# Performance work log

Hardware: AMD Instinct MI355X
Metric: run time of the kernel (lower is better)

The kernel has to match this reference:

```python
import jax, jax.numpy as jnp
import numpy as np

C = 256
CQK = C // 8  # reduction_ratio = 8


def setup_inputs() -> dict:
    key = jax.random.key(0)
    ks = jax.random.split(key, 8)
    B, H, W = 8, 64, 64
    x = jax.random.normal(ks[0], (B, C, H, W), dtype=jnp.float32)
    s_in = 1.0 / np.sqrt(C)
    Wq = jax.random.normal(ks[1], (CQK, C), dtype=jnp.float32) * s_in
    bq = jax.random.normal(ks[2], (CQK,), dtype=jnp.float32) * 0.01
    Wk = jax.random.normal(ks[3], (CQK, C), dtype=jnp.float32) * s_in
    bk = jax.random.normal(ks[4], (CQK,), dtype=jnp.float32) * 0.01
    Wv = jax.random.normal(ks[5], (C, C), dtype=jnp.float32) * s_in
    bv = jax.random.normal(ks[6], (C,), dtype=jnp.float32) * 0.01
    gamma = jax.random.normal(ks[7], (1,), dtype=jnp.float32) * 0.1
    return {"x": x, "Wq": Wq, "bq": bq, "Wk": Wk, "bk": bk,
            "Wv": Wv, "bv": bv, "gamma": gamma}


def reference(x, Wq, bq, Wk, bk, Wv, bv, gamma):
    B, Cc, H, W = x.shape
    N = H * W
    xf = x.reshape(B, Cc, N)  # [B, C, N]
    # 1x1 convs == per-pixel linear maps over channels
    q = jnp.einsum('qc,bcn->bnq', Wq, xf) + bq            # [B, N, Cqk]
    k = jnp.einsum('kc,bcn->bkn', Wk, xf) + bk[None, :, None]  # [B, Cqk, N]
    v = jnp.einsum('vc,bcn->bvn', Wv, xf) + bv[None, :, None]  # [B, C, N]
    # unscaled attention scores, softmax over keys (last dim)
    scores = jax.nn.softmax(jnp.einsum('bnq,bqm->bnm', q, k), axis=-1)  # [B, N, N]
    # out[b,c,n] = sum_m v[b,c,m] * scores[b,n,m]  (torch: value @ scores^T)
    attn = jnp.einsum('bvm,bnm->bvn', v, scores)          # [B, C, N]
    out = gamma[0] * attn.reshape(B, Cc, H, W) + x
    return out
```

## Files before the change

### kernel.cpp

```cpp
#include <hip/hip_runtime.h>

static constexpr int B_   = 8;
static constexpr int C_   = 256;
static constexpr int CQK_ = 32;
static constexpr int N_   = 4096;

typedef __attribute__((ext_vector_type(4)))  float f32x4;
typedef __attribute__((ext_vector_type(16))) float f32x16;
typedef __attribute__((ext_vector_type(8)))  short short8;
typedef __attribute__((ext_vector_type(2)))  unsigned int u32x2;
typedef unsigned short ushort_t;

__device__ inline unsigned short f2bf(float f) {
    unsigned u = __float_as_uint(f);
    return (unsigned short)((u + 0x7FFFu + ((u >> 16) & 1u)) >> 16);
}
__device__ inline unsigned packbf(float lo, float hi) {
    return (unsigned)f2bf(lo) | ((unsigned)f2bf(hi) << 16);
}
__device__ inline unsigned cvtpk(float lo, float hi) {
    unsigned r;
    asm("v_cvt_pk_bf16_f32 %0, %1, %2" : "=v"(r) : "v"(lo), "v"(hi));
    return r;
}
__device__ inline float vexp2(float x) {
    float r;
    asm("v_exp_f32 %0, %1" : "=v"(r) : "v"(x));
    return r;
}
__device__ inline void plswap(unsigned& a, unsigned& b) {
    asm("v_permlane32_swap_b32 %0, %1" : "+v"(a), "+v"(b));
}

__device__ inline int swzbits(int m) {
    return ((m & 3) << 5) | (((m >> 3) & 1) << 4);
}

template <int OFF>
__device__ inline u32x2 tr8(unsigned a) {
    u32x2 d;
    asm volatile("ds_read_b64_tr_b16 %0, %1 offset:%2"
                 : "=v"(d) : "v"(a), "i"(OFF));
    return d;
}

__device__ inline short8 mk8(u32x2 lo, u32x2 hi) {
    union { unsigned u[4]; short8 s; } v;
    v.u[0] = lo.x; v.u[1] = lo.y; v.u[2] = hi.x; v.u[3] = hi.y;
    return v.s;
}
__device__ inline short8 mk8u(unsigned a, unsigned b, unsigned c, unsigned d) {
    union { unsigned u[4]; short8 s; } v;
    v.u[0] = a; v.u[1] = b; v.u[2] = c; v.u[3] = d;
    return v.s;
}

__global__ __launch_bounds__(256) void prep_kernel(
    const float* __restrict__ Wq, const float* __restrict__ bq,
    const float* __restrict__ Wk, const float* __restrict__ bk,
    const float* __restrict__ Wv, const float* __restrict__ bv,
    ushort_t* __restrict__ Wall, float* __restrict__ ball)
{
    const int r = blockIdx.x;
    const int t = threadIdx.x;
    const float LOG2E = 1.4426950408889634f;
    const float* src;
    float bsrc, sc;
    if (r < 32)      { src = Wq + (size_t)r * C_;        bsrc = bq[r];      sc = LOG2E; }
    else if (r < 64) { src = Wk + (size_t)(r - 32) * C_; bsrc = bk[r - 32]; sc = 1.0f; }
    else             { src = Wv + (size_t)(r - 64) * C_; bsrc = bv[r - 64]; sc = 1.0f; }
    Wall[(size_t)r * C_ + t] = f2bf(src[t] * sc);
    if (t == 0) ball[r] = bsrc * sc;
}

__global__ __launch_bounds__(256) void proj_kernel(
    const float* __restrict__ x,
    const ushort_t* __restrict__ Wall, const float* __restrict__ ball,
    ushort_t* __restrict__ Qb, ushort_t* __restrict__ Kb, ushort_t* __restrict__ Vt)
{
    __shared__ __align__(16) unsigned char xs[C_ * 128];
    typedef __attribute__((address_space(3))) unsigned char lds_byte;
    const unsigned sbase = (unsigned)(size_t)(lds_byte*)xs;

    const int b  = blockIdx.x & 7;
    const int n0 = (blockIdx.x >> 3) << 6;
    const int t  = threadIdx.x;

    {
        const int cst = t >> 4;
        const int n4  = (t & 15) << 2;
        const float* xb = x + (size_t)b * C_ * N_ + n0;
        #pragma unroll
        for (int i = 0; i < 16; ++i) {
            const int c = 16 * i + cst;
            float4 v = *(const float4*)(xb + (size_t)c * N_ + n4);
            u32x2 pk;
            pk.x = packbf(v.x, v.y);
            pk.y = packbf(v.z, v.w);
            *(u32x2*)(xs + c * 128 + ((n4 * 2) ^ swzbits(c))) = pk;
        }
    }
    __syncthreads();

    const int l  = t & 63, w = t >> 6;
    const int li = l & 15, g = l >> 4;
    const int rr = li >> 2, ss = l & 3;
    const int swz_tr = (rr << 5) | ((g & 1) << 4);

    f32x4 acc[5][4];
    #pragma unroll
    for (int i = 0; i < 5; ++i)
        #pragma unroll
        for (int j = 0; j < 4; ++j) acc[i][j] = (f32x4){0.f, 0.f, 0.f, 0.f};

    #pragma unroll 2
    for (int kg = 0; kg < 8; ++kg) {
        u32x2 pb[4][2];
        #pragma unroll
        for (int jn = 0; jn < 4; ++jn) {
            unsigned a = sbase + (32 * kg + 8 * g + rr) * 128
                       + ((32 * jn + 8 * ss) ^ swz_tr);
            pb[jn][0] = tr8<0>(a);
            pb[jn][1] = tr8<512>(a);
        }
        short8 af[5];
        #pragma unroll
        for (int tm = 0; tm < 5; ++tm)
            af[tm] = *(const short8*)(Wall + (size_t)(16 * (4 * tm + w) + li) * C_
                                      + 32 * kg + 8 * g);
        asm volatile("s_waitcnt lgkmcnt(0)" ::: "memory");
        __builtin_amdgcn_sched_barrier(0);
        #pragma unroll
        for (int jn = 0; jn < 4; ++jn) {
            short8 Bf = mk8(pb[jn][0], pb[jn][1]);
            acc[0][jn] = __builtin_amdgcn_mfma_f32_16x16x32_bf16(
                             af[0], Bf, acc[0][jn], 0, 0, 0);
            #pragma unroll
            for (int tm = 1; tm < 5; ++tm)
                acc[tm][jn] = __builtin_amdgcn_mfma_f32_16x16x32_bf16(
                                  Bf, af[tm], acc[tm][jn], 0, 0, 0);
        }
    }

    {
        const int oc0 = 16 * w + 4 * g;
        float4 bias = *(const float4*)(ball + oc0);
        ushort_t* dst = (w < 2) ? Qb : Kb;
        const int col = (w < 2) ? oc0 : (oc0 - 32);
        #pragma unroll
        for (int jn = 0; jn < 4; ++jn) {
            const int n = n0 + 16 * jn + li;
            f32x4 a = acc[0][jn];
            u32x2 pk;
            pk.x = packbf(a[0] + bias.x, a[1] + bias.y);
            pk.y = packbf(a[2] + bias.z, a[3] + bias.w);
            *(u32x2*)(dst + (size_t)(b * N_ + n) * CQK_ + col) = pk;
        }
    }
    {
        const int sx = (li & 7) << 4;
        #pragma unroll
        for (int tm = 1; tm < 5; ++tm) {
            const int c  = 16 * (4 * tm + w) + li - 64;
            const float bc = ball[64 + c];
            char* vrow = (char*)Vt
                       + ((size_t)(b * 64 + (n0 >> 6)) * 256 + c) * 128;
            #pragma unroll
            for (int jn = 0; jn < 4; ++jn) {
                f32x4 a = acc[tm][jn];
                u32x2 pk;
                pk.x = packbf(a[0] + bc, a[1] + bc);
                pk.y = packbf(a[2] + bc, a[3] + bc);
                *(u32x2*)(vrow + ((32 * jn + 8 * g) ^ sx)) = pk;
            }
        }
    }
}

__global__ __launch_bounds__(256, 2) void attn_kernel(
    const float* __restrict__ x,
    const ushort_t* __restrict__ Qb, const ushort_t* __restrict__ Kb,
    const ushort_t* __restrict__ Vt,
    const float* __restrict__ gamma, float* __restrict__ out)
{
    __shared__ __align__(16) unsigned char smem[66560];

    const int b   = blockIdx.x & 7;
    const int n0  = (blockIdx.x >> 3) << 6;
    const int t   = threadIdx.x;
    const int l   = t & 63, w = t >> 6;
    const int l31 = l & 31, h2 = l >> 5;
    const int sxv = (l & 7) << 4;
    unsigned char* wlds = smem + w * 16384;
    float* rslw = (float*)(smem + 65536) + w * 64;

    short8 qfv[2][2];
    #pragma unroll
    for (int jq = 0; jq < 2; ++jq)
        #pragma unroll
        for (int kh = 0; kh < 2; ++kh)
            qfv[jq][kh] = *(const short8*)(Qb
                + (size_t)(b * N_ + n0 + 32 * jq + l31) * CQK_ + 16 * kh + 8 * h2);

    f32x16 acc[2][2];
    #pragma unroll
    for (int i = 0; i < 2; ++i)
        #pragma unroll
        for (int j = 0; j < 2; ++j)
            #pragma unroll
            for (int e = 0; e < 16; ++e) acc[i][j][e] = 0.f;
    float rs[2] = {0.f, 0.f};

    const ushort_t* Kbb = Kb + (size_t)(b * N_) * CQK_;
    const char* Vgb = (const char*)Vt + (size_t)b * 64 * 32768 + w * 8192;

    short8 kfA[2][2], kfB[2][2];

    #pragma unroll
    for (int jm = 0; jm < 2; ++jm)
        #pragma unroll
        for (int kh = 0; kh < 2; ++kh)
            kfA[jm][kh] = *(const short8*)(Kbb
                + (size_t)(32 * jm + l31) * CQK_ + 16 * kh + 8 * h2);
    #pragma unroll
    for (int i = 0; i < 8; ++i)
        __builtin_amdgcn_global_load_lds(
            (const __attribute__((address_space(1))) unsigned int*)(Vgb + l * 16 + i * 1024),
            (__attribute__((address_space(3))) unsigned int*)(wlds + l * 16 + i * 1024),
            16, 0, 0);

#define CHUNK_BODY(CH, KFC, KFN)                                                \
    {                                                                           \
        const int chn = ((CH) + 1) & 63;                                        \
                                                         \
        _Pragma("unroll")                                                       \
        for (int jm = 0; jm < 2; ++jm)                                          \
            _Pragma("unroll")                                                   \
            for (int kh = 0; kh < 2; ++kh)                                      \
                KFN[jm][kh] = *(const short8*)(Kbb                              \
                    + (size_t)(64 * chn + 32 * jm + l31) * CQK_                 \
                    + 16 * kh + 8 * h2);                                        \
                                 \
        {                                                                       \
            const char* gsrc = Vgb + (size_t)chn * 32768 + l * 16;              \
            unsigned char* ldst = wlds + (((CH) + 1) & 1) * 8192 + l * 16;      \
            _Pragma("unroll")                                                   \
            for (int i = 0; i < 8; ++i)                                         \
                __builtin_amdgcn_global_load_lds(                               \
                    (const __attribute__((address_space(1))) unsigned int*)(gsrc + i * 1024), \
                    (__attribute__((address_space(3))) unsigned int*)(ldst + i * 1024), \
                    16, 0, 0);                                                  \
        }                                                                       \
            \
        unsigned paw[4][2][4];                                                  \
        _Pragma("unroll")                                                       \
        for (int jm = 0; jm < 2; ++jm) {                                        \
            _Pragma("unroll")                                                   \
            for (int jq = 0; jq < 2; ++jq) {                                    \
                f32x16 sv;                                                      \
                _Pragma("unroll")                                               \
                for (int e = 0; e < 16; ++e) sv[e] = 0.f;                       \
                sv = __builtin_amdgcn_mfma_f32_32x32x16_bf16(                   \
                         KFC[jm][0], qfv[jq][0], sv, 0, 0, 0);                  \
                sv = __builtin_amdgcn_mfma_f32_32x32x16_bf16(                   \
                         KFC[jm][1], qfv[jq][1], sv, 0, 0, 0);                  \
                float ev[16];                                                   \
                _Pragma("unroll")                                               \
                for (int e = 0; e < 16; ++e) ev[e] = vexp2(sv[e]);              \
                float sm = ((ev[0] + ev[1]) + (ev[2] + ev[3]))                  \
                         + ((ev[4] + ev[5]) + (ev[6] + ev[7]))                  \
                         + ((ev[8] + ev[9]) + (ev[10] + ev[11]))                \
                         + ((ev[12] + ev[13]) + (ev[14] + ev[15]));             \
                rs[jq] += sm;                                                   \
                unsigned u0 = cvtpk(ev[0], ev[1]),   u1 = cvtpk(ev[2], ev[3]);  \
                unsigned u2 = cvtpk(ev[4], ev[5]),   u3 = cvtpk(ev[6], ev[7]);  \
                unsigned u4 = cvtpk(ev[8], ev[9]),   u5 = cvtpk(ev[10], ev[11]);\
                unsigned u6 = cvtpk(ev[12], ev[13]), u7 = cvtpk(ev[14], ev[15]);\
                plswap(u0, u2); plswap(u1, u3);                                 \
                plswap(u4, u6); plswap(u5, u7);                                 \
                paw[2 * jm + 0][jq][0] = u0; paw[2 * jm + 0][jq][1] = u1;       \
                paw[2 * jm + 0][jq][2] = u2; paw[2 * jm + 0][jq][3] = u3;       \
                paw[2 * jm + 1][jq][0] = u4; paw[2 * jm + 1][jq][1] = u5;       \
                paw[2 * jm + 1][jq][2] = u6; paw[2 * jm + 1][jq][3] = u7;       \
            }                                                                   \
        }                                                                       \
                \
        asm volatile("s_waitcnt vmcnt(12)" ::: "memory");                       \
                           \
        {                                                                       \
            const unsigned char* vb = wlds + ((CH) & 1) * 8192;                 \
            short8 vv[2][4];                                                    \
            _Pragma("unroll")                                                   \
            for (int jc = 0; jc < 2; ++jc)                                      \
                _Pragma("unroll")                                               \
                for (int s = 0; s < 4; ++s)                                     \
                    vv[jc][s] = *(const short8*)(vb + (32 * jc + l31) * 128     \
                                   + ((32 * s + 16 * h2) ^ sxv));               \
            _Pragma("unroll")                                                   \
            for (int jq = 0; jq < 2; ++jq)                                      \
                _Pragma("unroll")                                               \
                for (int jc = 0; jc < 2; ++jc)                                  \
                    _Pragma("unroll")                                           \
                    for (int s = 0; s < 4; ++s)                                 \
                        acc[jq][jc] = __builtin_amdgcn_mfma_f32_32x32x16_bf16(  \
                            mk8u(paw[s][jq][0], paw[s][jq][1],                  \
                                 paw[s][jq][2], paw[s][jq][3]),                 \
                            vv[jc][s], acc[jq][jc], 0, 0, 0);                   \
        }                                                                       \
    }

    for (int mc = 0; mc < 64; mc += 2) {
        CHUNK_BODY(mc,     kfA, kfB)
        CHUNK_BODY(mc + 1, kfB, kfA)
    }
#undef CHUNK_BODY

    #pragma unroll
    for (int jq = 0; jq < 2; ++jq)
        rs[jq] += __shfl_xor(rs[jq], 32, 64);
    if (l < 32) {
        rslw[l]      = rs[0];
        rslw[32 + l] = rs[1];
    }
    asm volatile("s_waitcnt lgkmcnt(0)" ::: "memory");

    const float gm = gamma[0];
    #pragma unroll
    for (int jq = 0; jq < 2; ++jq)
        #pragma unroll
        for (int rg = 0; rg < 4; ++rg) {
            f32x4 sv = *(const f32x4*)(rslw + 32 * jq + 8 * rg + 4 * h2);
            float i0 = 1.0f / sv[0], i1 = 1.0f / sv[1];
            float i2 = 1.0f / sv[2], i3 = 1.0f / sv[3];
            const int n = n0 + 32 * jq + 8 * rg + 4 * h2;
            #pragma unroll
            for (int jc = 0; jc < 2; ++jc) {
                const int c = 64 * w + 32 * jc + l31;
                const size_t rowoff = (size_t)(b * C_ + c) * N_ + n;
                float4 xv = *(const float4*)(x + rowoff);
                float4 o;
                o.x = gm * acc[jq][jc][4 * rg + 0] * i0 + xv.x;
                o.y = gm * acc[jq][jc][4 * rg + 1] * i1 + xv.y;
                o.z = gm * acc[jq][jc][4 * rg + 2] * i2 + xv.z;
                o.w = gm * acc[jq][jc][4 * rg + 3] * i3 + xv.w;
                *(float4*)(out + rowoff) = o;
            }
        }
}

extern "C" void kernel_launch(void* const* d_in, const int* in_sizes, int n_in,
                              void* d_out, int out_size, void* d_ws, size_t ws_size,
                              hipStream_t stream)
{
    const float* x     = (const float*)d_in[0];
    const float* Wq    = (const float*)d_in[1];
    const float* bq    = (const float*)d_in[2];
    const float* Wk    = (const float*)d_in[3];
    const float* bk    = (const float*)d_in[4];
    const float* Wv    = (const float*)d_in[5];
    const float* bv    = (const float*)d_in[6];
    const float* gamma = (const float*)d_in[7];
    float* out = (float*)d_out;

    ushort_t* ws = (ushort_t*)d_ws;
    ushort_t* Qb   = ws;
    ushort_t* Kb   = Qb + (size_t)B_ * N_ * CQK_;
    ushort_t* Vt   = Kb + (size_t)B_ * N_ * CQK_;
    ushort_t* Wall = Vt + (size_t)B_ * C_ * N_;
    float*    ball = (float*)(Wall + (size_t)320 * C_);

    prep_kernel<<<320, 256, 0, stream>>>(Wq, bq, Wk, bk, Wv, bv, Wall, ball);
    proj_kernel<<<B_ * (N_ / 64), 256, 0, stream>>>(x, Wall, ball, Qb, Kb, Vt);
    attn_kernel<<<B_ * (N_ / 64), 256, 0, stream>>>(x, Qb, Kb, Vt, gamma, out);
}
```

Measured before the change: 150.6 us.

## Halve attention query tile to 32 and re-layout V into 32-key chunks

The attention kernel now handles 32 queries per block instead of 64 and iterates over 128 key chunks of 32 instead of 64 chunks of 64. The grid doubles, LDS and register use per block halve, and the launch-bounds occupancy hint is dropped. The projection kernel writes V in a matching 32-key chunk layout with a new XOR swizzle. This trades reuse of each K/V chunk across queries, so K/V traffic and per-chunk overhead double, for more blocks and higher occupancy to hide latency.

```diff
diff --git a/kernel.cpp b/kernel.cpp
--- a/kernel.cpp
+++ b/kernel.cpp
@@ -157,73 +157,69 @@
             *(u32x2*)(dst + (size_t)(b * N_ + n) * CQK_ + col) = pk;
         }
     }
-    {
-        const int sx = (li & 7) << 4;
-        #pragma unroll
-        for (int tm = 1; tm < 5; ++tm) {
-            const int c  = 16 * (4 * tm + w) + li - 64;
-            const float bc = ball[64 + c];
-            char* vrow = (char*)Vt
-                       + ((size_t)(b * 64 + (n0 >> 6)) * 256 + c) * 128;
-            #pragma unroll
-            for (int jn = 0; jn < 4; ++jn) {
-                f32x4 a = acc[tm][jn];
-                u32x2 pk;
-                pk.x = packbf(a[0] + bc, a[1] + bc);
-                pk.y = packbf(a[2] + bc, a[3] + bc);
-                *(u32x2*)(vrow + ((32 * jn + 8 * g) ^ sx)) = pk;
-            }
-        }
-    }
-}
-
-__global__ __launch_bounds__(256, 2) void attn_kernel(
+    #pragma unroll
+    for (int tm = 1; tm < 5; ++tm) {
+        const int c  = 16 * (4 * tm + w) + li - 64;
+        const float bc = ball[64 + c];
+        const int sxc = ((c >> 1) & 3) << 4;
+        #pragma unroll
+        for (int jn = 0; jn < 4; ++jn) {
+            const int ch = (n0 >> 5) + (jn >> 1);
+            const int mcol = 32 * (jn & 1) + 8 * g;
+            f32x4 a = acc[tm][jn];
+            u32x2 pk;
+            pk.x = packbf(a[0] + bc, a[1] + bc);
+            pk.y = packbf(a[2] + bc, a[3] + bc);
+            char* dst = (char*)Vt + (size_t)(b * 128 + ch) * 16384
+                      + c * 64 + (mcol ^ sxc);
+            *(u32x2*)dst = pk;
+        }
+    }
+}
+
+__global__ __launch_bounds__(256) void attn_kernel(
     const float* __restrict__ x,
     const ushort_t* __restrict__ Qb, const ushort_t* __restrict__ Kb,
     const ushort_t* __restrict__ Vt,
     const float* __restrict__ gamma, float* __restrict__ out)
 {
-    __shared__ __align__(16) unsigned char smem[66560];
+    __shared__ __align__(16) unsigned char smem[33280];
 
     const int b   = blockIdx.x & 7;
-    const int n0  = (blockIdx.x >> 3) << 6;
+    const int n0  = (blockIdx.x >> 3) << 5;
     const int t   = threadIdx.x;
     const int l   = t & 63, w = t >> 6;
     const int l31 = l & 31, h2 = l >> 5;
-    const int sxv = (l & 7) << 4;
-    unsigned char* wlds = smem + w * 16384;
-    float* rslw = (float*)(smem + 65536) + w * 64;
-
-    short8 qfv[2][2];
-    #pragma unroll
-    for (int jq = 0; jq < 2; ++jq)
-        #pragma unroll
-        for (int kh = 0; kh < 2; ++kh)
-            qfv[jq][kh] = *(const short8*)(Qb
-                + (size_t)(b * N_ + n0 + 32 * jq + l31) * CQK_ + 16 * kh + 8 * h2);
-
-    f32x16 acc[2][2];
-    #pragma unroll
-    for (int i = 0; i < 2; ++i)
-        #pragma unroll
-        for (int j = 0; j < 2; ++j)
-            #pragma unroll
-            for (int e = 0; e < 16; ++e) acc[i][j][e] = 0.f;
-    float rs[2] = {0.f, 0.f};
+    const int sxv = ((l31 >> 1) & 3) << 4;
+    unsigned char* wlds = smem + w * 8192;
+    float* rslw = (float*)(smem + 32768) + w * 32;
+
+    short8 qfv[2];
+    #pragma unroll
+    for (int kh = 0; kh < 2; ++kh)
+        qfv[kh] = *(const short8*)(Qb
+            + (size_t)(b * N_ + n0 + l31) * CQK_ + 16 * kh + 8 * h2);
+
+    f32x16 acc[2];
+    #pragma unroll
+    for (int j = 0; j < 2; ++j)
+        #pragma unroll
+        for (int e = 0; e < 16; ++e) acc[j][e] = 0.f;
+    f32x16 zf16;
+    #pragma unroll
+    for (int e = 0; e < 16; ++e) zf16[e] = 0.f;
+    float rs = 0.f;
 
     const ushort_t* Kbb = Kb + (size_t)(b * N_) * CQK_;
-    const char* Vgb = (const char*)Vt + (size_t)b * 64 * 32768 + w * 8192;
-
-    short8 kfA[2][2], kfB[2][2];
-
-    #pragma unroll
-    for (int jm = 0; jm < 2; ++jm)
-        #pragma unroll
-        for (int kh = 0; kh < 2; ++kh)
-            kfA[jm][kh] = *(const short8*)(Kbb
-                + (size_t)(32 * jm + l31) * CQK_ + 16 * kh + 8 * h2);
-    #pragma unroll
-    for (int i = 0; i < 8; ++i)
+    const char* Vgb = (const char*)Vt + (size_t)b * 128 * 16384 + w * 4096;
+
+    short8 kfA[2], kfB[2];
+
+    #pragma unroll
+    for (int kh = 0; kh < 2; ++kh)
+        kfA[kh] = *(const short8*)(Kbb + (size_t)l31 * CQK_ + 16 * kh + 8 * h2);
+    #pragma unroll
+    for (int i = 0; i < 4; ++i)
         __builtin_amdgcn_global_load_lds(
             (const __attribute__((address_space(1))) unsigned int*)(Vgb + l * 16 + i * 1024),
             (__attribute__((address_space(3))) unsigned int*)(wlds + l * 16 + i * 1024),
@@ -231,121 +227,98 @@
 
 #define CHUNK_BODY(CH, KFC, KFN)                                                \
     {                                                                           \
-        const int chn = ((CH) + 1) & 63;                                        \
+        const int chn = ((CH) + 1) & 127;                                       \
                                                          \
         _Pragma("unroll")                                                       \
-        for (int jm = 0; jm < 2; ++jm)                                          \
-            _Pragma("unroll")                                                   \
-            for (int kh = 0; kh < 2; ++kh)                                      \
-                KFN[jm][kh] = *(const short8*)(Kbb                              \
-                    + (size_t)(64 * chn + 32 * jm + l31) * CQK_                 \
-                    + 16 * kh + 8 * h2);                                        \
+        for (int kh = 0; kh < 2; ++kh)                                          \
+            KFN[kh] = *(const short8*)(Kbb                                      \
+                + (size_t)(32 * chn + l31) * CQK_ + 16 * kh + 8 * h2);          \
                                  \
         {                                                                       \
-            const char* gsrc = Vgb + (size_t)chn * 32768 + l * 16;              \
-            unsigned char* ldst = wlds + (((CH) + 1) & 1) * 8192 + l * 16;      \
+            const char* gsrc = Vgb + (size_t)chn * 16384 + l * 16;              \
+            unsigned char* ldst = wlds + (((CH) + 1) & 1) * 4096 + l * 16;      \
             _Pragma("unroll")                                                   \
-            for (int i = 0; i < 8; ++i)                                         \
+            for (int i = 0; i < 4; ++i)                                         \
                 __builtin_amdgcn_global_load_lds(                               \
                     (const __attribute__((address_space(1))) unsigned int*)(gsrc + i * 1024), \
                     (__attribute__((address_space(3))) unsigned int*)(ldst + i * 1024), \
                     16, 0, 0);                                                  \
         }                                                                       \
             \
-        unsigned paw[4][2][4];                                                  \
-        _Pragma("unroll")                                                       \
-        for (int jm = 0; jm < 2; ++jm) {                                        \
+        unsigned paw[2][4];                                                     \
+        {                                                                       \
+            f32x16 sv = __builtin_amdgcn_mfma_f32_32x32x16_bf16(                \
+                            KFC[0], qfv[0], zf16, 0, 0, 0);                     \
+            sv = __builtin_amdgcn_mfma_f32_32x32x16_bf16(                       \
+                     KFC[1], qfv[1], sv, 0, 0, 0);                              \
+            float ev[16];                                                       \
             _Pragma("unroll")                                                   \
-            for (int jq = 0; jq < 2; ++jq) {                                    \
-                f32x16 sv;                                                      \
-                _Pragma("unroll")                                               \
-                for (int e = 0; e < 16; ++e) sv[e] = 0.f;                       \
-                sv = __builtin_amdgcn_mfma_f32_32x32x16_bf16(                   \
-                         KFC[jm][0], qfv[jq][0], sv, 0, 0, 0);                  \
-                sv = __builtin_amdgcn_mfma_f32_32x32x16_bf16(                   \
-                         KFC[jm][1], qfv[jq][1], sv, 0, 0, 0);                  \
-                float ev[16];                                                   \
-                _Pragma("unroll")                                               \
-                for (int e = 0; e < 16; ++e) ev[e] = vexp2(sv[e]);              \
-                float sm = ((ev[0] + ev[1]) + (ev[2] + ev[3]))                  \
-                         + ((ev[4] + ev[5]) + (ev[6] + ev[7]))                  \
-                         + ((ev[8] + ev[9]) + (ev[10] + ev[11]))                \
-                         + ((ev[12] + ev[13]) + (ev[14] + ev[15]));             \
-                rs[jq] += sm;                                                   \
-                unsigned u0 = cvtpk(ev[0], ev[1]),   u1 = cvtpk(ev[2], ev[3]);  \
-                unsigned u2 = cvtpk(ev[4], ev[5]),   u3 = cvtpk(ev[6], ev[7]);  \
-                unsigned u4 = cvtpk(ev[8], ev[9]),   u5 = cvtpk(ev[10], ev[11]);\
-                unsigned u6 = cvtpk(ev[12], ev[13]), u7 = cvtpk(ev[14], ev[15]);\
-                plswap(u0, u2); plswap(u1, u3);                                 \
-                plswap(u4, u6); plswap(u5, u7);                                 \
-                paw[2 * jm + 0][jq][0] = u0; paw[2 * jm + 0][jq][1] = u1;       \
-                paw[2 * jm + 0][jq][2] = u2; paw[2 * jm + 0][jq][3] = u3;       \
-                paw[2 * jm + 1][jq][0] = u4; paw[2 * jm + 1][jq][1] = u5;       \
-                paw[2 * jm + 1][jq][2] = u6; paw[2 * jm + 1][jq][3] = u7;       \
-            }                                                                   \
+            for (int e = 0; e < 16; ++e) ev[e] = vexp2(sv[e]);                  \
+            rs += (((ev[0] + ev[1]) + (ev[2] + ev[3]))                          \
+                 + ((ev[4] + ev[5]) + (ev[6] + ev[7])))                         \
+                + (((ev[8] + ev[9]) + (ev[10] + ev[11]))                        \
+                 + ((ev[12] + ev[13]) + (ev[14] + ev[15])));                    \
+            unsigned u0 = cvtpk(ev[0], ev[1]),   u1 = cvtpk(ev[2], ev[3]);      \
+            unsigned u2 = cvtpk(ev[4], ev[5]),   u3 = cvtpk(ev[6], ev[7]);      \
+            unsigned u4 = cvtpk(ev[8], ev[9]),   u5 = cvtpk(ev[10], ev[11]);    \
+            unsigned u6 = cvtpk(ev[12], ev[13]), u7 = cvtpk(ev[14], ev[15]);    \
+            plswap(u0, u2); plswap(u1, u3);                                     \
+            plswap(u4, u6); plswap(u5, u7);                                     \
+            paw[0][0] = u0; paw[0][1] = u1; paw[0][2] = u2; paw[0][3] = u3;     \
+            paw[1][0] = u4; paw[1][1] = u5; paw[1][2] = u6; paw[1][3] = u7;     \
         }                                                                       \
                 \
-        asm volatile("s_waitcnt vmcnt(12)" ::: "memory");                       \
+        asm volatile("s_waitcnt vmcnt(6)" ::: "memory");                        \
                            \
         {                                                                       \
-            const unsigned char* vb = wlds + ((CH) & 1) * 8192;                 \
-            short8 vv[2][4];                                                    \
+            const unsigned char* vb = wlds + ((CH) & 1) * 4096;                 \
+            short8 vv[2][2];                                                    \
             _Pragma("unroll")                                                   \
             for (int jc = 0; jc < 2; ++jc)                                      \
                 _Pragma("unroll")                                               \
-                for (int s = 0; s < 4; ++s)                                     \
-                    vv[jc][s] = *(const short8*)(vb + (32 * jc + l31) * 128     \
+                for (int s = 0; s < 2; ++s)                                     \
+                    vv[jc][s] = *(const short8*)(vb + (32 * jc + l31) * 64      \
                                    + ((32 * s + 16 * h2) ^ sxv));               \
             _Pragma("unroll")                                                   \
-            for (int jq = 0; jq < 2; ++jq)                                      \
+            for (int jc = 0; jc < 2; ++jc)                                      \
                 _Pragma("unroll")                                               \
-                for (int jc = 0; jc < 2; ++jc)                                  \
-                    _Pragma("unroll")                                           \
-                    for (int s = 0; s < 4; ++s)                                 \
-                        acc[jq][jc] = __builtin_amdgcn_mfma_f32_32x32x16_bf16(  \
-                            mk8u(paw[s][jq][0], paw[s][jq][1],                  \
-                                 paw[s][jq][2], paw[s][jq][3]),                 \
-                            vv[jc][s], acc[jq][jc], 0, 0, 0);                   \
+                for (int s = 0; s < 2; ++s)                                     \
+                    acc[jc] = __builtin_amdgcn_mfma_f32_32x32x16_bf16(          \
+                        mk8u(paw[s][0], paw[s][1], paw[s][2], paw[s][3]),       \
+                        vv[jc][s], acc[jc], 0, 0, 0);                           \
         }                                                                       \
     }
 
-    for (int mc = 0; mc < 64; mc += 2) {
+    for (int mc = 0; mc < 128; mc += 2) {
         CHUNK_BODY(mc,     kfA, kfB)
         CHUNK_BODY(mc + 1, kfB, kfA)
     }
 #undef CHUNK_BODY
 
-    #pragma unroll
-    for (int jq = 0; jq < 2; ++jq)
-        rs[jq] += __shfl_xor(rs[jq], 32, 64);
-    if (l < 32) {
-        rslw[l]      = rs[0];
-        rslw[32 + l] = rs[1];
-    }
+    rs += __shfl_xor(rs, 32, 64);
+    if (l < 32) rslw[l31] = rs;
     asm volatile("s_waitcnt lgkmcnt(0)" ::: "memory");
 
     const float gm = gamma[0];
     #pragma unroll
-    for (int jq = 0; jq < 2; ++jq)
-        #pragma unroll
-        for (int rg = 0; rg < 4; ++rg) {
-            f32x4 sv = *(const f32x4*)(rslw + 32 * jq + 8 * rg + 4 * h2);
-            float i0 = 1.0f / sv[0], i1 = 1.0f / sv[1];
-            float i2 = 1.0f / sv[2], i3 = 1.0f / sv[3];
-            const int n = n0 + 32 * jq + 8 * rg + 4 * h2;
-            #pragma unroll
-            for (int jc = 0; jc < 2; ++jc) {
-                const int c = 64 * w + 32 * jc + l31;
-                const size_t rowoff = (size_t)(b * C_ + c) * N_ + n;
-                float4 xv = *(const float4*)(x + rowoff);
-                float4 o;
-                o.x = gm * acc[jq][jc][4 * rg + 0] * i0 + xv.x;
-                o.y = gm * acc[jq][jc][4 * rg + 1] * i1 + xv.y;
-                o.z = gm * acc[jq][jc][4 * rg + 2] * i2 + xv.z;
-                o.w = gm * acc[jq][jc][4 * rg + 3] * i3 + xv.w;
-                *(float4*)(out + rowoff) = o;
-            }
-        }
+    for (int rg = 0; rg < 4; ++rg) {
+        f32x4 sv = *(const f32x4*)(rslw + 8 * rg + 4 * h2);
+        float i0 = 1.0f / sv[0], i1 = 1.0f / sv[1];
+        float i2 = 1.0f / sv[2], i3 = 1.0f / sv[3];
+        const int n = n0 + 8 * rg + 4 * h2;
+        #pragma unroll
+        for (int jc = 0; jc < 2; ++jc) {
+            const int c = 64 * w + 32 * jc + l31;
+            const size_t rowoff = (size_t)(b * C_ + c) * N_ + n;
+            float4 xv = *(const float4*)(x + rowoff);
+            float4 o;
+            o.x = gm * acc[jc][4 * rg + 0] * i0 + xv.x;
+            o.y = gm * acc[jc][4 * rg + 1] * i1 + xv.y;
+            o.z = gm * acc[jc][4 * rg + 2] * i2 + xv.z;
+            o.w = gm * acc[jc][4 * rg + 3] * i3 + xv.w;
+            *(float4*)(out + rowoff) = o;
+        }
+    }
 }
 
 extern "C" void kernel_launch(void* const* d_in, const int* in_sizes, int n_in,
@@ -371,5 +344,5 @@
 
     prep_kernel<<<320, 256, 0, stream>>>(Wq, bq, Wk, bk, Wv, bv, Wall, ball);
     proj_kernel<<<B_ * (N_ / 64), 256, 0, stream>>>(x, Wall, ball, Qb, Kb, Vt);
-    attn_kernel<<<B_ * (N_ / 64), 256, 0, stream>>>(x, Qb, Kb, Vt, gamma, out);
-}
+    attn_kernel<<<B_ * (N_ / 32), 256, 0, stream>>>(x, Qb, Kb, Vt, gamma, out);
+}
```

Result: slower. 189.5 us (+25.9%).

## Split attention work across waves by key half instead of channel slice

Applied to the files above, without the earlier changes.

Each wave now takes half of each 64-key chunk and 128 output channels, instead of all keys and 64 channels. This halves the redundant QK^T MFMA and exp work per wave, since each score is computed once rather than by all four waves. The V layout written by the projection kernel changes to match, and the two key-halves are reduced through shared memory at the end. The cost is doubled accumulator registers (acc[2][4]), extra LDS traffic, two barriers, and an epilogue handled by only half the waves.

```diff
diff --git a/kernel.cpp b/kernel.cpp
--- a/kernel.cpp
+++ b/kernel.cpp
@@ -157,22 +157,25 @@
             *(u32x2*)(dst + (size_t)(b * N_ + n) * CQK_ + col) = pk;
         }
     }
-    {
-        const int sx = (li & 7) << 4;
-        #pragma unroll
-        for (int tm = 1; tm < 5; ++tm) {
-            const int c  = 16 * (4 * tm + w) + li - 64;
-            const float bc = ball[64 + c];
-            char* vrow = (char*)Vt
-                       + ((size_t)(b * 64 + (n0 >> 6)) * 256 + c) * 128;
-            #pragma unroll
-            for (int jn = 0; jn < 4; ++jn) {
-                f32x4 a = acc[tm][jn];
-                u32x2 pk;
-                pk.x = packbf(a[0] + bc, a[1] + bc);
-                pk.y = packbf(a[2] + bc, a[3] + bc);
-                *(u32x2*)(vrow + ((32 * jn + 8 * g) ^ sx)) = pk;
-            }
+    #pragma unroll
+    for (int tm = 1; tm < 5; ++tm) {
+        const int c  = 16 * (4 * tm + w) + li - 64;
+        const float bc = ball[64 + c];
+        const int ch = c >> 7;
+        const int cl = c & 127;
+        const int X  = (c & 3) ^ ((c >> 2) & 3);
+        char* qbase = (char*)Vt + ((size_t)(b * 64 + (n0 >> 6)) * 4 + 2 * ch) * 8192
+                    + cl * 64;
+        #pragma unroll
+        for (int jn = 0; jn < 4; ++jn) {
+            const int mp = 16 * jn + 4 * g;
+            const int mh = mp >> 5;
+            const int jg = (mp & 31) >> 3;
+            f32x4 a = acc[tm][jn];
+            u32x2 pk;
+            pk.x = packbf(a[0] + bc, a[1] + bc);
+            pk.y = packbf(a[2] + bc, a[3] + bc);
+            *(u32x2*)(qbase + mh * 8192 + 16 * (jg ^ X) + 8 * (g & 1)) = pk;
         }
     }
 }
@@ -190,9 +193,10 @@
     const int t   = threadIdx.x;
     const int l   = t & 63, w = t >> 6;
     const int l31 = l & 31, h2 = l >> 5;
-    const int sxv = (l & 7) << 4;
+    const int mh  = w & 1,  ch = w >> 1;
+    const int sxv = ((l31 & 3) ^ ((l31 >> 2) & 3)) << 4;
     unsigned char* wlds = smem + w * 16384;
-    float* rslw = (float*)(smem + 65536) + w * 64;
+    float* rstab = (float*)(smem + 65536);
 
     short8 qfv[2][2];
     #pragma unroll
@@ -202,26 +206,28 @@
             qfv[jq][kh] = *(const short8*)(Qb
                 + (size_t)(b * N_ + n0 + 32 * jq + l31) * CQK_ + 16 * kh + 8 * h2);
 
-    f32x16 acc[2][2];
+    f32x16 acc[2][4];
     #pragma unroll
     for (int i = 0; i < 2; ++i)
         #pragma unroll
-        for (int j = 0; j < 2; ++j)
+        for (int j = 0; j < 4; ++j)
             #pragma unroll
             for (int e = 0; e < 16; ++e) acc[i][j][e] = 0.f;
+    f32x16 zf16;
+    #pragma unroll
+    for (int e = 0; e < 16; ++e) zf16[e] = 0.f;
     float rs[2] = {0.f, 0.f};
 
     const ushort_t* Kbb = Kb + (size_t)(b * N_) * CQK_;
-    const char* Vgb = (const char*)Vt + (size_t)b * 64 * 32768 + w * 8192;
-
-    short8 kfA[2][2], kfB[2][2];
-
-    #pragma unroll
-    for (int jm = 0; jm < 2; ++jm)
-        #pragma unroll
-        for (int kh = 0; kh < 2; ++kh)
-            kfA[jm][kh] = *(const short8*)(Kbb
-                + (size_t)(32 * jm + l31) * CQK_ + 16 * kh + 8 * h2);
+    const char* Vgb = (const char*)Vt + (size_t)b * 64 * 32768
+                    + (2 * ch + mh) * 8192;
+
+    short8 kfA[2], kfB[2];
+
+    #pragma unroll
+    for (int kh = 0; kh < 2; ++kh)
+        kfA[kh] = *(const short8*)(Kbb + (size_t)(32 * mh + l31) * CQK_
+                                   + 16 * kh + 8 * h2);
     #pragma unroll
     for (int i = 0; i < 8; ++i)
         __builtin_amdgcn_global_load_lds(
@@ -232,15 +238,12 @@
 #define CHUNK_BODY(CH, KFC, KFN)                                                \
     {                                                                           \
         const int chn = ((CH) + 1) & 63;                                        \
-                                                         \
+                                              \
         _Pragma("unroll")                                                       \
-        for (int jm = 0; jm < 2; ++jm)                                          \
-            _Pragma("unroll")                                                   \
-            for (int kh = 0; kh < 2; ++kh)                                      \
-                KFN[jm][kh] = *(const short8*)(Kbb                              \
-                    + (size_t)(64 * chn + 32 * jm + l31) * CQK_                 \
-                    + 16 * kh + 8 * h2);                                        \
-                                 \
+        for (int kh = 0; kh < 2; ++kh)                                          \
+            KFN[kh] = *(const short8*)(Kbb                                      \
+                + (size_t)(64 * chn + 32 * mh + l31) * CQK_ + 16 * kh + 8 * h2);\
+                    \
         {                                                                       \
             const char* gsrc = Vgb + (size_t)chn * 32768 + l * 16;              \
             unsigned char* ldst = wlds + (((CH) + 1) & 1) * 8192 + l * 16;      \
@@ -251,61 +254,54 @@
                     (__attribute__((address_space(3))) unsigned int*)(ldst + i * 1024), \
                     16, 0, 0);                                                  \
         }                                                                       \
-            \
-        unsigned paw[4][2][4];                                                  \
+                     \
+        unsigned paw[2][2][4];                                                  \
         _Pragma("unroll")                                                       \
-        for (int jm = 0; jm < 2; ++jm) {                                        \
+        for (int jq = 0; jq < 2; ++jq) {                                        \
+            f32x16 sv = __builtin_amdgcn_mfma_f32_32x32x16_bf16(                \
+                            KFC[0], qfv[jq][0], zf16, 0, 0, 0);                 \
+            sv = __builtin_amdgcn_mfma_f32_32x32x16_bf16(                       \
+                     KFC[1], qfv[jq][1], sv, 0, 0, 0);                          \
+            float ev[16];                                                       \
             _Pragma("unroll")                                                   \
-            for (int jq = 0; jq < 2; ++jq) {                                    \
-                f32x16 sv;                                                      \
-                _Pragma("unroll")                                               \
-                for (int e = 0; e < 16; ++e) sv[e] = 0.f;                       \
-                sv = __builtin_amdgcn_mfma_f32_32x32x16_bf16(                   \
-                         KFC[jm][0], qfv[jq][0], sv, 0, 0, 0);                  \
-                sv = __builtin_amdgcn_mfma_f32_32x32x16_bf16(                   \
-                         KFC[jm][1], qfv[jq][1], sv, 0, 0, 0);                  \
-                float ev[16];                                                   \
-                _Pragma("unroll")                                               \
-                for (int e = 0; e < 16; ++e) ev[e] = vexp2(sv[e]);              \
-                float sm = ((ev[0] + ev[1]) + (ev[2] + ev[3]))                  \
-                         + ((ev[4] + ev[5]) + (ev[6] + ev[7]))                  \
-                         + ((ev[8] + ev[9]) + (ev[10] + ev[11]))                \
-                         + ((ev[12] + ev[13]) + (ev[14] + ev[15]));             \
-                rs[jq] += sm;                                                   \
-                unsigned u0 = cvtpk(ev[0], ev[1]),   u1 = cvtpk(ev[2], ev[3]);  \
-                unsigned u2 = cvtpk(ev[4], ev[5]),   u3 = cvtpk(ev[6], ev[7]);  \
-                unsigned u4 = cvtpk(ev[8], ev[9]),   u5 = cvtpk(ev[10], ev[11]);\
-                unsigned u6 = cvtpk(ev[12], ev[13]), u7 = cvtpk(ev[14], ev[15]);\
-                plswap(u0, u2); plswap(u1, u3);                                 \
-                plswap(u4, u6); plswap(u5, u7);                                 \
-                paw[2 * jm + 0][jq][0] = u0; paw[2 * jm + 0][jq][1] = u1;       \
-                paw[2 * jm + 0][jq][2] = u2; paw[2 * jm + 0][jq][3] = u3;       \
-                paw[2 * jm + 1][jq][0] = u4; paw[2 * jm + 1][jq][1] = u5;       \
-                paw[2 * jm + 1][jq][2] = u6; paw[2 * jm + 1][jq][3] = u7;       \
-            }                                                                   \
+            for (int e = 0; e < 16; ++e) ev[e] = vexp2(sv[e]);                  \
+            rs[jq] += (((ev[0] + ev[1]) + (ev[2] + ev[3]))                      \
+                     + ((ev[4] + ev[5]) + (ev[6] + ev[7])))                     \
+                    + (((ev[8] + ev[9]) + (ev[10] + ev[11]))                    \
+                     + ((ev[12] + ev[13]) + (ev[14] + ev[15])));                \
+            unsigned u0 = cvtpk(ev[0], ev[1]),   u1 = cvtpk(ev[2], ev[3]);      \
+            unsigned u2 = cvtpk(ev[4], ev[5]),   u3 = cvtpk(ev[6], ev[7]);      \
+            unsigned u4 = cvtpk(ev[8], ev[9]),   u5 = cvtpk(ev[10], ev[11]);    \
+            unsigned u6 = cvtpk(ev[12], ev[13]), u7 = cvtpk(ev[14], ev[15]);    \
+            plswap(u0, u2); plswap(u1, u3);                                     \
+            plswap(u4, u6); plswap(u5, u7);                                     \
+            paw[jq][0][0] = u0; paw[jq][0][1] = u1;                             \
+            paw[jq][0][2] = u2; paw[jq][0][3] = u3;                             \
+            paw[jq][1][0] = u4; paw[jq][1][1] = u5;                             \
+            paw[jq][1][2] = u6; paw[jq][1][3] = u7;                             \
         }                                                                       \
                 \
-        asm volatile("s_waitcnt vmcnt(12)" ::: "memory");                       \
-                           \
+        asm volatile("s_waitcnt vmcnt(10)" ::: "memory");                       \
+               \
         {                                                                       \
             const unsigned char* vb = wlds + ((CH) & 1) * 8192;                 \
-            short8 vv[2][4];                                                    \
             _Pragma("unroll")                                                   \
-            for (int jc = 0; jc < 2; ++jc)                                      \
+            for (int s = 0; s < 2; ++s) {                                       \
+                short8 vv[4];                                                   \
                 _Pragma("unroll")                                               \
-                for (int s = 0; s < 4; ++s)                                     \
-                    vv[jc][s] = *(const short8*)(vb + (32 * jc + l31) * 128     \
+                for (int jc = 0; jc < 4; ++jc)                                  \
+                    vv[jc] = *(const short8*)(vb + (32 * jc + l31) * 64         \
                                    + ((32 * s + 16 * h2) ^ sxv));               \
-            _Pragma("unroll")                                                   \
-            for (int jq = 0; jq < 2; ++jq)                                      \
                 _Pragma("unroll")                                               \
-                for (int jc = 0; jc < 2; ++jc)                                  \
+                for (int jq = 0; jq < 2; ++jq) {                                \
+                    short8 A = mk8u(paw[jq][s][0], paw[jq][s][1],               \
+                                    paw[jq][s][2], paw[jq][s][3]);              \
                     _Pragma("unroll")                                           \
-                    for (int s = 0; s < 4; ++s)                                 \
+                    for (int jc = 0; jc < 4; ++jc)                              \
                         acc[jq][jc] = __builtin_amdgcn_mfma_f32_32x32x16_bf16(  \
-                            mk8u(paw[s][jq][0], paw[s][jq][1],                  \
-                                 paw[s][jq][2], paw[s][jq][3]),                 \
-                            vv[jc][s], acc[jq][jc], 0, 0, 0);                   \
+                                          A, vv[jc], acc[jq][jc], 0, 0, 0);     \
+                }                                                               \
+            }                                                                   \
         }                                                                       \
     }
 
@@ -319,33 +315,76 @@
     for (int jq = 0; jq < 2; ++jq)
         rs[jq] += __shfl_xor(rs[jq], 32, 64);
     if (l < 32) {
-        rslw[l]      = rs[0];
-        rslw[32 + l] = rs[1];
-    }
-    asm volatile("s_waitcnt lgkmcnt(0)" ::: "memory");
-
-    const float gm = gamma[0];
-    #pragma unroll
-    for (int jq = 0; jq < 2; ++jq)
-        #pragma unroll
-        for (int rg = 0; rg < 4; ++rg) {
-            f32x4 sv = *(const f32x4*)(rslw + 32 * jq + 8 * rg + 4 * h2);
-            float i0 = 1.0f / sv[0], i1 = 1.0f / sv[1];
-            float i2 = 1.0f / sv[2], i3 = 1.0f / sv[3];
-            const int n = n0 + 32 * jq + 8 * rg + 4 * h2;
+        rstab[(w * 2 + 0) * 32 + l31] = rs[0];
+        rstab[(w * 2 + 1) * 32 + l31] = rs[1];
+    }
+    asm volatile("s_waitcnt vmcnt(0)" ::: "memory");
+    __syncthreads();
+
+    if (mh == 1) {
+        float* dst = (float*)(smem + ch * 32768);
+        #pragma unroll
+        for (int jq = 0; jq < 2; ++jq)
             #pragma unroll
-            for (int jc = 0; jc < 2; ++jc) {
-                const int c = 64 * w + 32 * jc + l31;
-                const size_t rowoff = (size_t)(b * C_ + c) * N_ + n;
-                float4 xv = *(const float4*)(x + rowoff);
-                float4 o;
-                o.x = gm * acc[jq][jc][4 * rg + 0] * i0 + xv.x;
-                o.y = gm * acc[jq][jc][4 * rg + 1] * i1 + xv.y;
-                o.z = gm * acc[jq][jc][4 * rg + 2] * i2 + xv.z;
-                o.w = gm * acc[jq][jc][4 * rg + 3] * i3 + xv.w;
-                *(float4*)(out + rowoff) = o;
+            for (int jc = 0; jc < 4; ++jc) {
+                float* tb = dst + (jq * 4 + jc) * 1024 + l * 16;
+                #pragma unroll
+                for (int e4 = 0; e4 < 4; ++e4) {
+                    f32x4 p;
+                    p[0] = acc[jq][jc][4 * e4 + 0];
+                    p[1] = acc[jq][jc][4 * e4 + 1];
+                    p[2] = acc[jq][jc][4 * e4 + 2];
+                    p[3] = acc[jq][jc][4 * e4 + 3];
+                    *(f32x4*)(tb + 4 * (e4 ^ (l & 3))) = p;
+                }
             }
-        }
+    }
+    __syncthreads();
+
+    if (mh == 0) {
+        const float* src = (const float*)(smem + ch * 32768);
+        #pragma unroll
+        for (int jq = 0; jq < 2; ++jq)
+            #pragma unroll
+            for (int jc = 0; jc < 4; ++jc) {
+                const float* tb = src + (jq * 4 + jc) * 1024 + l * 16;
+                #pragma unroll
+                for (int e4 = 0; e4 < 4; ++e4) {
+                    f32x4 p = *(const f32x4*)(tb + 4 * (e4 ^ (l & 3)));
+                    acc[jq][jc][4 * e4 + 0] += p[0];
+                    acc[jq][jc][4 * e4 + 1] += p[1];
+                    acc[jq][jc][4 * e4 + 2] += p[2];
+                    acc[jq][jc][4 * e4 + 3] += p[3];
+                }
+            }
+        const float gm = gamma[0];
+        #pragma unroll
+        for (int jq = 0; jq < 2; ++jq)
+            #pragma unroll
+            for (int rg = 0; rg < 4; ++rg) {
+                f32x4 s0 = *(const f32x4*)(rstab + (w * 2 + jq) * 32
+                                           + 8 * rg + 4 * h2);
+                f32x4 s1 = *(const f32x4*)(rstab + ((w + 1) * 2 + jq) * 32
+                                           + 8 * rg + 4 * h2);
+                float i0 = 1.0f / (s0[0] + s1[0]);
+                float i1 = 1.0f / (s0[1] + s1[1]);
+                float i2 = 1.0f / (s0[2] + s1[2]);
+                float i3 = 1.0f / (s0[3] + s1[3]);
+                const int n = n0 + 32 * jq + 8 * rg + 4 * h2;
+                #pragma unroll
+                for (int jc = 0; jc < 4; ++jc) {
+                    const int c = 128 * ch + 32 * jc + l31;
+                    const size_t rowoff = (size_t)(b * C_ + c) * N_ + n;
+                    float4 xv = *(const float4*)(x + rowoff);
+                    float4 o;
+                    o.x = gm * acc[jq][jc][4 * rg + 0] * i0 + xv.x;
+                    o.y = gm * acc[jq][jc][4 * rg + 1] * i1 + xv.y;
+                    o.z = gm * acc[jq][jc][4 * rg + 2] * i2 + xv.z;
+                    o.w = gm * acc[jq][jc][4 * rg + 3] * i3 + xv.w;
+                    *(float4*)(out + rowoff) = o;
+                }
+            }
+    }
 }
 
 extern "C" void kernel_launch(void* const* d_in, const int* in_sizes, int n_in,
```

New measurement: 138.0 us. 8.4% less time.
